# Optimization experiments

Hardware: AMD Instinct MI355X
Metric: run time of the kernel (lower is better)

The kernel has to match this reference:

```python
import jax, jax.numpy as jnp
import numpy as np

T = 4096          # total packed tokens (4 docs x 1024)
NUM_DOCS = 4
H = 16            # n_heads
D = 64            # head_dim == v_head_dim
TOPK = 64         # per-token top-k KV selection (<= min doc len)


def setup_inputs() -> dict:
    key = jax.random.key(0)
    kq, kk, kv, ki, ks = jax.random.split(key, 5)
    q = jax.random.normal(kq, (T, H, D), dtype=jnp.float32)
    k = jax.random.normal(kk, (T, H, D), dtype=jnp.float32)
    v = jax.random.normal(kv, (T, H, D), dtype=jnp.float32)
    # 4 equal-length documents of 1024 tokens
    cu_seqlens = (jnp.arange(NUM_DOCS + 1, dtype=jnp.int32) * (T // NUM_DOCS))
    # global top-k indices; reference clamps them into the owning document
    topk_indices = jax.random.randint(ki, (T, TOPK), 0, T, dtype=jnp.int32)
    # selector scores in (0,1), like indexer softmax outputs
    topk_scores = jax.random.uniform(ks, (T, TOPK), dtype=jnp.float32)
    return {
        "q_packed": q,
        "k_packed": k,
        "v_packed": v,
        "cu_seqlens": cu_seqlens,
        "topk_indices": topk_indices,
        "topk_scores": topk_scores,
    }


def reference(q_packed, k_packed, v_packed, cu_seqlens, topk_indices, topk_scores):
    total_tokens, n_heads, head_dim = q_packed.shape
    scale = head_dim ** -0.5

    # Per-token document assignment (vectorized replacement for the doc loop).
    tok = jnp.arange(total_tokens, dtype=cu_seqlens.dtype)
    seg = jnp.searchsorted(cu_seqlens[1:], tok, side="right")  # (T,) doc id
    start = cu_seqlens[seg]                                    # (T,)
    seq_len = cu_seqlens[seg + 1] - start                      # (T,)

    # Localize and clamp top-k indices into the owning document, then
    # convert back to global packed indices for gathering.
    local = jnp.clip(topk_indices - start[:, None], 0, (seq_len - 1)[:, None])
    gidx = start[:, None] + local                              # (T, K)

    k_gathered = k_packed[gidx]   # (T, K, H, D)
    v_gathered = v_packed[gidx]   # (T, K, H, D)

    # q . k_sel, softmax over the k selected keys
    scores = jnp.einsum("thd,tkhd->thk", q_packed, k_gathered) * scale
    w = jax.nn.softmax(scores, axis=-1)                        # (T, H, K)

    # Modulate by selector scores (head-shared) and renormalize.
    w = w * topk_scores[:, None, :]
    w = w / (jnp.sum(w, axis=-1, keepdims=True) + 1e-12)

    out = jnp.einsum("thk,tkhd->thd", w, v_gathered)           # (T, H, D)
    return out
```

## Files before the change

kernel.cpp:

```cpp
#include <hip/hip_runtime.h>
#include <hip/hip_fp16.h>


#define T_TOK 4096
#define NH    16
#define HD    64
#define KSEL  64
#define KV_ELEMS (T_TOK * NH * HD)

typedef _Float16 h2v __attribute__((ext_vector_type(2)));

static __device__ __forceinline__ h2v u2h2v(unsigned u) {
    return __builtin_bit_cast(h2v, u);
}
static __device__ __forceinline__ __half2 u2h2(unsigned u) {
    return __builtin_bit_cast(__half2, u);
}
static __device__ __forceinline__ unsigned h22u(__half2 h) {
    return __builtin_bit_cast(unsigned, h);
}
static __device__ __forceinline__ h2v f2h2v(float a, float b) {
    __half2 t = __floats2half2_rn(a, b);
    return __builtin_bit_cast(h2v, t);
}

__global__ __launch_bounds__(256) void cvt_fp16(
    const float4* __restrict__ kM, const float4* __restrict__ vM,
    uint2* __restrict__ kH, uint2* __restrict__ vH)
{
    const int n4 = KV_ELEMS / 4;
    const int i  = blockIdx.x * blockDim.x + threadIdx.x;
    const bool isK = i < n4;
    const float4 f = isK ? kM[i] : vM[i - n4];
    __half2 lo = __floats2half2_rn(f.x, f.y);
    __half2 hi = __floats2half2_rn(f.z, f.w);
    uint2 u;
    u.x = h22u(lo);
    u.y = h22u(hi);
    if (isK) kH[i] = u; else vH[i - n4] = u;
}

__global__ __launch_bounds__(256) void dsa_sparse_attn(
    const float*  __restrict__ qM,
    const __half* __restrict__ kH,
    const __half* __restrict__ vH,
    const int*    __restrict__ cu,
    const int*    __restrict__ tidx,
    const float*  __restrict__ tsc,
    float*        __restrict__ out,
    int num_docs)
{
    __shared__ uint4 sV[4][512];

    const int wave = threadIdx.x >> 6;
    const int lane = threadIdx.x & 63;

    const int b            = blockIdx.x;
    const int xcd          = b & 7;
    const int j            = b >> 3;
    const int token_block  = j & 255;
    const int slice_within = j >> 8;
    const int s            = xcd + (slice_within << 3);
    const int h            = s & (NH - 1);
    const int t            = (s >> 4) * (T_TOK / 4) + token_block * 4 + wave;
    const int gid          = t * NH + h;

    int seg = 0;
    for (int i = 1; i < num_docs; ++i)
        if (t >= cu[i]) seg = i;
    const int start = cu[seg];
    const int len   = cu[seg + 1] - start;

    int idx = tidx[t * KSEL + lane];
    int loc = idx - start;
    loc = loc < 0 ? 0 : loc;
    loc = loc > len - 1 ? len - 1 : loc;
    const int g = start + loc;
    const float sc = tsc[t * KSEL + lane];

    const int laneCol = lane & 3;
    const int laneRow = lane >> 2;
    const int laneQ8  = lane >> 3;
    const int laneC8  = lane & 7;

    const uint4* kf = (const uint4*)kH;
    const int hc1 = h * 8 + laneCol;

    {
        const __half* vbase = vH;
        #pragma unroll
        for (int i = 0; i < 8; ++i) {
            const int gr = __shfl(g, i * 8 + laneQ8, 64);
            const __half* gp = vbase + ((gr * NH + h) << 6) + (laneC8 << 3);
            __builtin_amdgcn_global_load_lds(
                (const __attribute__((address_space(1))) unsigned int*)gp,
                (__attribute__((address_space(3))) unsigned int*)&sV[wave][i * 64],
                16, 0, 0);
        }
    }

    const float4* qv = (const float4*)(qM + gid * HD);
    const float4 f0 = qv[laneCol * 2];
    const float4 f1 = qv[laneCol * 2 + 1];
    const float4 f2 = qv[8 + laneCol * 2];
    const float4 f3 = qv[8 + laneCol * 2 + 1];
    h2v qa[4] = { f2h2v(f0.x, f0.y), f2h2v(f0.z, f0.w),
                  f2h2v(f1.x, f1.y), f2h2v(f1.z, f1.w) };
    h2v qb[4] = { f2h2v(f2.x, f2.y), f2h2v(f2.z, f2.w),
                  f2h2v(f3.x, f3.y), f2h2v(f3.z, f3.w) };

    float score = 0.f;
    #pragma unroll
    for (int rg = 0; rg < 4; ++rg) {
        const int grow = __shfl(g, rg * 16 + laneRow, 64);
        const uint4 kA = kf[grow * 128 + hc1];
        const uint4 kB = kf[grow * 128 + hc1 + 4];
        float p = 0.f;
        p = __builtin_amdgcn_fdot2(u2h2v(kA.x), qa[0], p, false);
        p = __builtin_amdgcn_fdot2(u2h2v(kA.y), qa[1], p, false);
        p = __builtin_amdgcn_fdot2(u2h2v(kA.z), qa[2], p, false);
        p = __builtin_amdgcn_fdot2(u2h2v(kA.w), qa[3], p, false);
        p = __builtin_amdgcn_fdot2(u2h2v(kB.x), qb[0], p, false);
        p = __builtin_amdgcn_fdot2(u2h2v(kB.y), qb[1], p, false);
        p = __builtin_amdgcn_fdot2(u2h2v(kB.z), qb[2], p, false);
        p = __builtin_amdgcn_fdot2(u2h2v(kB.w), qb[3], p, false);
        p += __shfl_xor(p, 1, 64);
        p += __shfl_xor(p, 2, 64);
        const float got = __shfl(p, (lane & 15) << 2, 64);
        if (rg == (lane >> 4)) score = got;
    }
    score *= 0.125f;

    const float e = __expf(score);
    const float p = e * sc;
    const unsigned hb  = (unsigned)__builtin_bit_cast(unsigned short, __float2half(p));
    const unsigned ppk = hb | (hb << 16);

    asm volatile("s_waitcnt vmcnt(0)" ::: "memory");
    __half2 acc[4];
    acc[0] = u2h2(0u); acc[1] = u2h2(0u); acc[2] = u2h2(0u); acc[3] = u2h2(0u);
    #pragma unroll
    for (int i = 0; i < 8; ++i) {
        const unsigned pu = (unsigned)__shfl((int)ppk, i * 8 + laneQ8, 64);
        const __half2 pk2 = u2h2(pu);
        const uint4 vv = sV[wave][i * 64 + lane];
        acc[0] = __hfma2(pk2, u2h2(vv.x), acc[0]);
        acc[1] = __hfma2(pk2, u2h2(vv.y), acc[1]);
        acc[2] = __hfma2(pk2, u2h2(vv.z), acc[2]);
        acc[3] = __hfma2(pk2, u2h2(vv.w), acc[3]);
    }

    float S2 = p;
    #pragma unroll
    for (int off = 32; off; off >>= 1)
        S2 += __shfl_xor(S2, off, 64);

    #pragma unroll
    for (int off = 8; off <= 32; off <<= 1) {
        #pragma unroll
        for (int jj = 0; jj < 4; ++jj) {
            const unsigned o = (unsigned)__shfl_xor((int)h22u(acc[jj]), off, 64);
            acc[jj] = __hadd2(acc[jj], u2h2(o));
        }
    }

    if (laneQ8 == 0) {
        const float inv = __builtin_amdgcn_rcpf(S2);
        const float2 a0 = __half22float2(acc[0]);
        const float2 a1 = __half22float2(acc[1]);
        const float2 a2 = __half22float2(acc[2]);
        const float2 a3 = __half22float2(acc[3]);
        float4* op = (float4*)(out + gid * HD + laneC8 * 8);
        op[0] = make_float4(a0.x * inv, a0.y * inv, a1.x * inv, a1.y * inv);
        op[1] = make_float4(a2.x * inv, a2.y * inv, a3.x * inv, a3.y * inv);
    }
}

extern "C" void kernel_launch(void* const* d_in, const int* in_sizes, int n_in,
                              void* d_out, int out_size, void* d_ws, size_t ws_size,
                              hipStream_t stream) {
    const float* q   = (const float*)d_in[0];
    const float* k   = (const float*)d_in[1];
    const float* v   = (const float*)d_in[2];
    const int*   cu  = (const int*)d_in[3];
    const int*   ti  = (const int*)d_in[4];
    const float* ts  = (const float*)d_in[5];
    float*       out = (float*)d_out;
    const int num_docs = in_sizes[3] - 1;

    __half* kH = (__half*)d_ws;
    __half* vH = kH + KV_ELEMS;

    const int n4 = KV_ELEMS / 4;
    hipLaunchKernelGGL(cvt_fp16, dim3(2 * n4 / 256), dim3(256), 0, stream,
                       (const float4*)k, (const float4*)v,
                       (uint2*)kH, (uint2*)vH);

    const int total_waves = T_TOK * NH;
    hipLaunchKernelGGL(dsa_sparse_attn, dim3(total_waves / 4), dim3(256), 0,
                       stream, q, (const __half*)kH, (const __half*)vH,
                       cu, ti, ts, out, num_docs);
}
```

Measured before the change: 155.3 us.

## Fuse QK and PV into one register loop with DPP/swizzle reductions

The score and value-accumulation phases now run in a single loop over key groups. Each 8-lane group owns one selected key row and loads that row's K and V straight into registers, which removes the LDS staging of V, the async global-to-LDS copies and the score broadcast shuffles. Cross-lane reductions for the dot products, the weight sum and the output accumulators now use DPP and ds_swizzle instead of generic shuffles. The trade-off is that V loads are no longer issued early to overlap with the QK phase, so latency hiding now depends on the compiler scheduling the unrolled loads.

```diff
diff --git a/kernel.cpp b/kernel.cpp
--- a/kernel.cpp
+++ b/kernel.cpp
@@ -16,12 +16,31 @@
 static __device__ __forceinline__ __half2 u2h2(unsigned u) {
     return __builtin_bit_cast(__half2, u);
 }
-static __device__ __forceinline__ unsigned h22u(__half2 h) {
-    return __builtin_bit_cast(unsigned, h);
-}
 static __device__ __forceinline__ h2v f2h2v(float a, float b) {
     __half2 t = __floats2half2_rn(a, b);
     return __builtin_bit_cast(h2v, t);
+}
+
+template<int CTRL>
+static __device__ __forceinline__ float dpp_addf(float x) {
+    const int s = __builtin_amdgcn_update_dpp(
+        0, __builtin_bit_cast(int, x), CTRL, 0xF, 0xF, true);
+    return x + __builtin_bit_cast(float, s);
+}
+
+template<int IMM>
+static __device__ __forceinline__ float swz_addf(float x) {
+    const int s = __builtin_amdgcn_ds_swizzle(__builtin_bit_cast(int, x), IMM);
+    return x + __builtin_bit_cast(float, s);
+}
+template<int IMM>
+static __device__ __forceinline__ __half2 swz_hadd2(__half2 x) {
+    const int s = __builtin_amdgcn_ds_swizzle(__builtin_bit_cast(int, x), IMM);
+    return __hadd2(x, __builtin_bit_cast(__half2, s));
+}
+static __device__ __forceinline__ __half2 sh32_hadd2(__half2 x) {
+    const int s = __shfl_xor(__builtin_bit_cast(int, x), 32, 64);
+    return __hadd2(x, __builtin_bit_cast(__half2, s));
 }
 
 __global__ __launch_bounds__(256) void cvt_fp16(
@@ -35,8 +54,8 @@
     __half2 lo = __floats2half2_rn(f.x, f.y);
     __half2 hi = __floats2half2_rn(f.z, f.w);
     uint2 u;
-    u.x = h22u(lo);
-    u.y = h22u(hi);
+    u.x = __builtin_bit_cast(unsigned, lo);
+    u.y = __builtin_bit_cast(unsigned, hi);
     if (isK) kH[i] = u; else vH[i - n4] = u;
 }
 
@@ -50,8 +69,6 @@
     float*        __restrict__ out,
     int num_docs)
 {
-    __shared__ uint4 sV[4][512];
-
     const int wave = threadIdx.x >> 6;
     const int lane = threadIdx.x & 63;
 
@@ -76,100 +93,70 @@
     loc = loc < 0 ? 0 : loc;
     loc = loc > len - 1 ? len - 1 : loc;
     const int g = start + loc;
-    const float sc = tsc[t * KSEL + lane];
 
-    const int laneCol = lane & 3;
-    const int laneRow = lane >> 2;
-    const int laneQ8  = lane >> 3;
-    const int laneC8  = lane & 7;
+    const int laneQ8 = lane >> 3;
+    const int laneC8 = lane & 7;
+
+    const float4* qv = (const float4*)(qM + gid * HD);
+    const float4 fA = qv[laneC8 * 2];
+    const float4 fB = qv[laneC8 * 2 + 1];
+    const h2v q0 = f2h2v(fA.x, fA.y);
+    const h2v q1 = f2h2v(fA.z, fA.w);
+    const h2v q2 = f2h2v(fB.x, fB.y);
+    const h2v q3 = f2h2v(fB.z, fB.w);
 
     const uint4* kf = (const uint4*)kH;
-    const int hc1 = h * 8 + laneCol;
+    const uint4* vf = (const uint4*)vH;
+    const float* scb = tsc + t * KSEL;
 
-    {
-        const __half* vbase = vH;
-        #pragma unroll
-        for (int i = 0; i < 8; ++i) {
-            const int gr = __shfl(g, i * 8 + laneQ8, 64);
-            const __half* gp = vbase + ((gr * NH + h) << 6) + (laneC8 << 3);
-            __builtin_amdgcn_global_load_lds(
-                (const __attribute__((address_space(1))) unsigned int*)gp,
-                (__attribute__((address_space(3))) unsigned int*)&sV[wave][i * 64],
-                16, 0, 0);
-        }
+    float S2part = 0.f;
+    __half2 acc0 = u2h2(0u), acc1 = u2h2(0u), acc2 = u2h2(0u), acc3 = u2h2(0u);
+
+    #pragma unroll
+    for (int rg = 0; rg < 8; ++rg) {
+        const int row = rg * 8 + laneQ8;
+        const int gr  = __shfl(g, row, 64);
+        const int base = (gr * NH + h) * 8 + laneC8;
+        const uint4 kk = kf[base];
+        const uint4 vv = vf[base];
+        const float sck = scb[row];
+
+        float p = 0.f;
+        p = __builtin_amdgcn_fdot2(u2h2v(kk.x), q0, p, false);
+        p = __builtin_amdgcn_fdot2(u2h2v(kk.y), q1, p, false);
+        p = __builtin_amdgcn_fdot2(u2h2v(kk.z), q2, p, false);
+        p = __builtin_amdgcn_fdot2(u2h2v(kk.w), q3, p, false);
+        p = dpp_addf<0xB1>(p);
+        p = dpp_addf<0x4E>(p);
+        p = dpp_addf<0x141>(p);
+
+        const float w = __expf(p * 0.125f) * sck;
+        S2part += w;
+        const __half2 w2 = __floats2half2_rn(w, w);
+        acc0 = __hfma2(w2, u2h2(vv.x), acc0);
+        acc1 = __hfma2(w2, u2h2(vv.y), acc1);
+        acc2 = __hfma2(w2, u2h2(vv.z), acc2);
+        acc3 = __hfma2(w2, u2h2(vv.w), acc3);
     }
 
-    const float4* qv = (const float4*)(qM + gid * HD);
-    const float4 f0 = qv[laneCol * 2];
-    const float4 f1 = qv[laneCol * 2 + 1];
-    const float4 f2 = qv[8 + laneCol * 2];
-    const float4 f3 = qv[8 + laneCol * 2 + 1];
-    h2v qa[4] = { f2h2v(f0.x, f0.y), f2h2v(f0.z, f0.w),
-                  f2h2v(f1.x, f1.y), f2h2v(f1.z, f1.w) };
-    h2v qb[4] = { f2h2v(f2.x, f2.y), f2h2v(f2.z, f2.w),
-                  f2h2v(f3.x, f3.y), f2h2v(f3.z, f3.w) };
+    float S2 = S2part;
+    S2 = dpp_addf<0x140>(S2);
+    S2 = swz_addf<0x401F>(S2);
+    S2 += __shfl_xor(S2, 32, 64);
 
-    float score = 0.f;
-    #pragma unroll
-    for (int rg = 0; rg < 4; ++rg) {
-        const int grow = __shfl(g, rg * 16 + laneRow, 64);
-        const uint4 kA = kf[grow * 128 + hc1];
-        const uint4 kB = kf[grow * 128 + hc1 + 4];
-        float p = 0.f;
-        p = __builtin_amdgcn_fdot2(u2h2v(kA.x), qa[0], p, false);
-        p = __builtin_amdgcn_fdot2(u2h2v(kA.y), qa[1], p, false);
-        p = __builtin_amdgcn_fdot2(u2h2v(kA.z), qa[2], p, false);
-        p = __builtin_amdgcn_fdot2(u2h2v(kA.w), qa[3], p, false);
-        p = __builtin_amdgcn_fdot2(u2h2v(kB.x), qb[0], p, false);
-        p = __builtin_amdgcn_fdot2(u2h2v(kB.y), qb[1], p, false);
-        p = __builtin_amdgcn_fdot2(u2h2v(kB.z), qb[2], p, false);
-        p = __builtin_amdgcn_fdot2(u2h2v(kB.w), qb[3], p, false);
-        p += __shfl_xor(p, 1, 64);
-        p += __shfl_xor(p, 2, 64);
-        const float got = __shfl(p, (lane & 15) << 2, 64);
-        if (rg == (lane >> 4)) score = got;
-    }
-    score *= 0.125f;
-
-    const float e = __expf(score);
-    const float p = e * sc;
-    const unsigned hb  = (unsigned)__builtin_bit_cast(unsigned short, __float2half(p));
-    const unsigned ppk = hb | (hb << 16);
-
-    asm volatile("s_waitcnt vmcnt(0)" ::: "memory");
-    __half2 acc[4];
-    acc[0] = u2h2(0u); acc[1] = u2h2(0u); acc[2] = u2h2(0u); acc[3] = u2h2(0u);
-    #pragma unroll
-    for (int i = 0; i < 8; ++i) {
-        const unsigned pu = (unsigned)__shfl((int)ppk, i * 8 + laneQ8, 64);
-        const __half2 pk2 = u2h2(pu);
-        const uint4 vv = sV[wave][i * 64 + lane];
-        acc[0] = __hfma2(pk2, u2h2(vv.x), acc[0]);
-        acc[1] = __hfma2(pk2, u2h2(vv.y), acc[1]);
-        acc[2] = __hfma2(pk2, u2h2(vv.z), acc[2]);
-        acc[3] = __hfma2(pk2, u2h2(vv.w), acc[3]);
-    }
-
-    float S2 = p;
-    #pragma unroll
-    for (int off = 32; off; off >>= 1)
-        S2 += __shfl_xor(S2, off, 64);
-
-    #pragma unroll
-    for (int off = 8; off <= 32; off <<= 1) {
-        #pragma unroll
-        for (int jj = 0; jj < 4; ++jj) {
-            const unsigned o = (unsigned)__shfl_xor((int)h22u(acc[jj]), off, 64);
-            acc[jj] = __hadd2(acc[jj], u2h2(o));
-        }
-    }
+    acc0 = swz_hadd2<0x201F>(acc0); acc1 = swz_hadd2<0x201F>(acc1);
+    acc2 = swz_hadd2<0x201F>(acc2); acc3 = swz_hadd2<0x201F>(acc3);
+    acc0 = swz_hadd2<0x401F>(acc0); acc1 = swz_hadd2<0x401F>(acc1);
+    acc2 = swz_hadd2<0x401F>(acc2); acc3 = swz_hadd2<0x401F>(acc3);
+    acc0 = sh32_hadd2(acc0); acc1 = sh32_hadd2(acc1);
+    acc2 = sh32_hadd2(acc2); acc3 = sh32_hadd2(acc3);
 
     if (laneQ8 == 0) {
         const float inv = __builtin_amdgcn_rcpf(S2);
-        const float2 a0 = __half22float2(acc[0]);
-        const float2 a1 = __half22float2(acc[1]);
-        const float2 a2 = __half22float2(acc[2]);
-        const float2 a3 = __half22float2(acc[3]);
+        const float2 a0 = __half22float2(acc0);
+        const float2 a1 = __half22float2(acc1);
+        const float2 a2 = __half22float2(acc2);
+        const float2 a3 = __half22float2(acc3);
         float4* op = (float4*)(out + gid * HD + laneC8 * 8);
         op[0] = make_float4(a0.x * inv, a0.y * inv, a1.x * inv, a1.y * inv);
         op[1] = make_float4(a2.x * inv, a2.y * inv, a3.x * inv, a3.y * inv);
```

After: 144.3 us. -7.1%, faster.
